# Kernel optimization log

Hardware: AMD Instinct MI355X
Metric: run time of the kernel (lower is better)

## Reference

```python
import jax, jax.numpy as jnp
import numpy as np

B, N, D, U = 8, 2048, 512, 512

def setup_inputs() -> dict:
    key = jax.random.key(0)
    ks = jax.random.split(key, 7)
    s = 1.0 / np.sqrt(D)
    return {
        "inputs": jax.random.normal(ks[0], (B, N, D), dtype=jnp.float32),
        "Wq": jax.random.normal(ks[1], (D, U), dtype=jnp.float32) * s,
        "bq": jnp.zeros((U,), dtype=jnp.float32),
        "Wk": jax.random.normal(ks[2], (D, U), dtype=jnp.float32) * s,
        "bk": jnp.zeros((U,), dtype=jnp.float32),
        "Wv": jax.random.normal(ks[3], (D, U), dtype=jnp.float32) * s,
        "bv": jnp.zeros((U,), dtype=jnp.float32),
    }

def reference(inputs, Wq, bq, Wk, bk, Wv, bv):
    # Dense projections (Keras Dense: x @ W + b)
    Q = inputs @ Wq + bq  # [B, N, U]
    K = inputs @ Wk + bk  # [B, N, U]
    V = inputs @ Wv + bv  # [B, N, U]
    # NOTE: original module has NO 1/sqrt(d) scaling
    scores = jnp.einsum("bnu,bmu->bnm", Q, K)  # [B, N, N]
    attn = jax.nn.softmax(scores, axis=-1)
    return jnp.einsum("bnm,bmu->bnu", attn, V)  # [B, N, U]
```

## Files before the change

### kernel.cpp

```cpp
#include <hip/hip_runtime.h>


typedef _Float16 f16;
typedef _Float16 f16x4 __attribute__((ext_vector_type(4)));
typedef _Float16 f16x8 __attribute__((ext_vector_type(8)));
typedef float f32x4 __attribute__((ext_vector_type(4)));
typedef short s16x8 __attribute__((ext_vector_type(8)));
typedef unsigned short u16;

#define OFS 96.0f

__device__ __forceinline__ void stage16(const void* g, void* lds_uniform) {
    __builtin_amdgcn_global_load_lds(
        (const __attribute__((address_space(1))) void*)g,
        (__attribute__((address_space(3))) void*)lds_uniform,
        16, 0, 0);
}

__device__ __forceinline__ unsigned lds_off(const void* p) {
    return (unsigned)(size_t)(const __attribute__((address_space(3))) void*)p;
}

__device__ __forceinline__ f16x8 dsread16(unsigned a) {
    f16x8 r;
    asm volatile("ds_read_b128 %0, %1" : "=v"(r) : "v"(a));
    return r;
}
__device__ __forceinline__ s16x8 dsread16b(unsigned a) {
    s16x8 r;
    asm volatile("ds_read_b128 %0, %1" : "=v"(r) : "v"(a));
    return r;
}

__device__ __forceinline__ u16 f2bf(float f) {
    unsigned u = __builtin_bit_cast(unsigned, f);
    u = (u + 0x7FFF + ((u >> 16) & 1)) >> 16;
    return (u16)u;
}
__device__ __forceinline__ float bf2f(u16 b) {
    return __builtin_bit_cast(float, (unsigned)b << 16);
}

__global__ __launch_bounds__(256) void prep_fused(
    const float* __restrict__ X,
    const float* __restrict__ Wq, const float* __restrict__ Wk,
    const float* __restrict__ Wv,
    const float* __restrict__ bq, const float* __restrict__ bk,
    const float* __restrict__ bv,
    f16* __restrict__ X16, f16* __restrict__ Wt, float* __restrict__ biases) {
    __shared__ float t[32][33];
    const int bid = blockIdx.x, tid = threadIdx.x;
    if (bid < 8192) {
        int i = (bid * 256 + tid) * 4;
        float4 v = *(const float4*)(X + i);
        f16x4 o;
        o[0] = (f16)v.x; o[1] = (f16)v.y; o[2] = (f16)v.z; o[3] = (f16)v.w;
        *(f16x4*)(X16 + i) = o;
    } else if (bid < 8960) {
        int id = bid - 8192;
        int z = id >> 8, rem = id & 255;
        int u0 = (rem & 15) * 32, d0 = (rem >> 4) * 32;
        const float* W = (z == 0) ? Wq : (z == 1 ? Wk : Wv);
        f16* outp = Wt + (size_t)z * 262144;
        int tx = tid & 31, ty = tid >> 5;
#pragma unroll
        for (int r = 0; r < 4; r++)
            t[ty + 8 * r][tx] = W[(size_t)(d0 + ty + 8 * r) * 512 + u0 + tx];
        __syncthreads();
#pragma unroll
        for (int r = 0; r < 4; r++)
            outp[(size_t)(u0 + ty + 8 * r) * 512 + d0 + tx] = (f16)t[tx][ty + 8 * r];
    } else {
#pragma unroll
        for (int j = 0; j < 6; j++) {
            int i = j * 256 + tid;
            float v = (i < 512) ? bq[i] : (i < 1024) ? bk[i - 512] : bv[i - 1024];
            biases[i] = v;
        }
    }
}

template <int MODE>
__device__ __forceinline__ void gemm_core(
    const u16* __restrict__ A, int lda,
    const u16* __restrict__ Bt, int ldb,
    int m0, int n0, int K,
    const float* __restrict__ bias,
    void* __restrict__ Cv, int ldc,
    u16* As, u16* Bs) {
    __shared__ float rowbuf[128];

    const int tid = threadIdx.x;
    const int wid = tid >> 6, lane = tid & 63;

    if (MODE == 2) {
        if (tid < 128) rowbuf[tid] = bias[m0 + tid];
    }

    const int schunk = (lane & 7) ^ ((lane >> 3) & 7);
    const u16* gA = A + (size_t)(m0 + wid * 32 + (lane >> 3)) * lda + schunk * 8;
    const u16* gB = Bt + (size_t)(n0 + wid * 32 + (lane >> 3)) * ldb + schunk * 8;
    u16* ldsA = As + (wid * 32) * 64;
    u16* ldsB = Bs + (wid * 32) * 64;

    const int wr = wid >> 1, wc = wid & 1;
    const int frow = lane & 15;
    const int f7 = frow & 7;
    const int c_lo = (lane >> 4) ^ f7;
    const int c_hi = ((lane >> 4) | 4) ^ f7;
    const u16* fA_lo = As + (wr * 64 + frow) * 64 + c_lo * 8;
    const u16* fA_hi = As + (wr * 64 + frow) * 64 + c_hi * 8;
    const u16* fB_lo = Bs + (wc * 64 + frow) * 64 + c_lo * 8;
    const u16* fB_hi = Bs + (wc * 64 + frow) * 64 + c_hi * 8;

    f32x4 acc[4][4] = {};

    for (int kt = 0; kt < K; kt += 64) {
#pragma unroll
        for (int j = 0; j < 4; j++)
            stage16(gA + (size_t)(j * 8) * lda, ldsA + (j * 8) * 64);
#pragma unroll
        for (int j = 0; j < 4; j++)
            stage16(gB + (size_t)(j * 8) * ldb, ldsB + (j * 8) * 64);
        gA += 64; gB += 64;
        __syncthreads();

#pragma unroll
        for (int half = 0; half < 2; half++) {
            const u16* pA = half ? fA_hi : fA_lo;
            const u16* pB = half ? fB_hi : fB_lo;
            f16x8 af[4], bf[4];
#pragma unroll
            for (int i = 0; i < 4; i++) af[i] = *(const f16x8*)(const f16*)(pA + i * 16 * 64);
#pragma unroll
            for (int i = 0; i < 4; i++) bf[i] = *(const f16x8*)(const f16*)(pB + i * 16 * 64);
#pragma unroll
            for (int mi = 0; mi < 4; mi++)
#pragma unroll
                for (int ni = 0; ni < 4; ni++)
                    acc[mi][ni] = __builtin_amdgcn_mfma_f32_16x16x32_f16(
                        af[mi], bf[ni], acc[mi][ni], 0, 0, 0);
        }
        __syncthreads();
    }

    const int crow0 = m0 + wr * 64 + ((lane >> 4) << 2);
    const int ccol0 = n0 + wc * 64 + (lane & 15);

    if (MODE == 1) {
        f16* C = (f16*)Cv;
#pragma unroll
        for (int mi = 0; mi < 4; mi++)
#pragma unroll
            for (int ni = 0; ni < 4; ni++) {
                float cb = bias[ccol0 + ni * 16];
#pragma unroll
                for (int r = 0; r < 4; r++)
                    C[(size_t)(crow0 + mi * 16 + r) * ldc + ccol0 + ni * 16] =
                        (f16)(acc[mi][ni][r] + cb);
            }
    } else {
        u16* C = (u16*)Cv;
#pragma unroll
        for (int mi = 0; mi < 4; mi++)
#pragma unroll
            for (int ni = 0; ni < 4; ni++)
#pragma unroll
                for (int r = 0; r < 4; r++) {
                    float rb = rowbuf[crow0 + mi * 16 + r - m0];
                    C[(size_t)(crow0 + mi * 16 + r) * ldc + ccol0 + ni * 16] =
                        f2bf(acc[mi][ni][r] + rb);
                }
    }
}

__global__ __launch_bounds__(256, 3) void proj_fused(
    const u16* __restrict__ X16, const u16* __restrict__ Wt,
    const float* __restrict__ biases,
    u16* __restrict__ QK, u16* __restrict__ Vt) {
    __shared__ __align__(16) u16 As[128 * 64];
    __shared__ __align__(16) u16 Bs[128 * 64];
    const int bid = blockIdx.x;
    if (bid < 1024) {
        int z = bid >> 9, rem = bid & 511;
        int bx = rem & 127, by = rem >> 7;
        gemm_core<1>(X16, 512, Wt + (size_t)z * 262144, 512,
                     bx * 128, by * 128, 512,
                     biases + z * 512,
                     QK + (size_t)z * 8388608, 512, As, Bs);
    } else {
        int id = bid - 1024;
        int bz = id & 7, rem = id >> 3;
        int bx = rem & 3, by = rem >> 2;
        gemm_core<2>(Wt + (size_t)2 * 262144, 512,
                     X16 + (size_t)bz * 1048576, 512,
                     bx * 128, by * 128, 512,
                     biases + 1024,
                     Vt + (size_t)bz * 1048576, 2048, As, Bs);
    }
}

__global__ __launch_bounds__(512, 2) void score_gemm(
    const u16* __restrict__ Q, const u16* __restrict__ Kk,
    u16* __restrict__ P, float* __restrict__ rsp) {
    extern __shared__ __align__(16) char smem[];

    const int i = blockIdx.x;
    const int z = i & 7, y = (i >> 3) & 7, x = i >> 6;
    const int m0 = x * 256, n0 = y * 256;
    const u16* A  = Q  + (size_t)z * 1048576;
    const u16* Bt = Kk + (size_t)z * 1048576;
    u16* C = P + (size_t)z * 4194304;
    float* rs = rsp + ((size_t)z * 8 + y) * 8192;

    const int tid = threadIdx.x;
    const int wid = tid >> 6, lane = tid & 63;

    const int srow = lane >> 3;
    const int schunk = (lane & 7) ^ srow;
    const u16* gA0 = A  + (size_t)m0 * 512 + schunk * 8;
    const u16* gB0 = Bt + (size_t)n0 * 512 + schunk * 8;
    char* ldsbase = smem;

    auto stage_unit = [&](int u, int T, int b) {
        const u16* gm = (u < 2) ? gA0 : gB0;
        int rbase = (u & 1) * 128 + wid * 16;
        const u16* g = gm + (size_t)(rbase + srow) * 512 + T * 64;
        char* l = ldsbase + ((u < 2) ? 0 : 65536) + b * 32768 + rbase * 128;
        stage16(g, l);
        stage16(g + (size_t)8 * 512, l + 8 * 128);
    };

    const int wr = wid >> 2, wc = wid & 3;
    const int frow = lane & 15;
    const int f7 = frow & 7;
    const int c_lo = (lane >> 4) ^ f7;
    const int c_hi = ((lane >> 4) | 4) ^ f7;
    const unsigned smemB = lds_off(smem);
    const unsigned offA_lo = (unsigned)(((wr * 128 + frow) * 64 + c_lo * 8) * 2);
    const unsigned offA_hi = (unsigned)(((wr * 128 + frow) * 64 + c_hi * 8) * 2);
    const unsigned offB_lo = (unsigned)(((wc * 64 + frow) * 64 + c_lo * 8) * 2);
    const unsigned offB_hi = (unsigned)(((wc * 64 + frow) * 64 + c_hi * 8) * 2);

    f32x4 acc[8][4] = {};

    stage_unit(0, 0, 0); stage_unit(1, 0, 0);
    stage_unit(2, 0, 0); stage_unit(3, 0, 0);
    asm volatile("s_waitcnt vmcnt(0)" ::: "memory");
    asm volatile("s_barrier" ::: "memory");

#pragma unroll
    for (int T = 0; T < 8; ++T) {
        const int buf = T & 1;
        const unsigned baseA = smemB + (unsigned)(buf * 32768);
        const unsigned baseB = smemB + 65536u + (unsigned)(buf * 32768);

        f16x8 bf[4];
#pragma unroll
        for (int p = 0; p < 4; ++p) {
            const int kh = p >> 1, mh = p & 1;
            const unsigned aoff = baseA + (kh ? offA_hi : offA_lo);
            if (mh == 0) {
                const unsigned boff = baseB + (kh ? offB_hi : offB_lo);
#pragma unroll
                for (int ni = 0; ni < 4; ni++)
                    bf[ni] = dsread16(boff + (unsigned)(ni * 2048));
            }
            f16x8 af[4];
#pragma unroll
            for (int j = 0; j < 4; j++)
                af[j] = dsread16(aoff + (unsigned)((4 * mh + j) * 2048));

            if (T < 7) {
                if (p == 0) { stage_unit(0, T + 1, buf ^ 1); stage_unit(1, T + 1, buf ^ 1); }
                if (p == 1) { stage_unit(2, T + 1, buf ^ 1); stage_unit(3, T + 1, buf ^ 1); }
            }

            asm volatile("s_waitcnt lgkmcnt(0)" ::: "memory");
            __builtin_amdgcn_sched_barrier(0);
            __builtin_amdgcn_s_setprio(1);
#pragma unroll
            for (int j = 0; j < 4; j++)
#pragma unroll
                for (int ni = 0; ni < 4; ni++)
                    acc[4 * mh + j][ni] = __builtin_amdgcn_mfma_f32_16x16x32_f16(
                        af[j], bf[ni], acc[4 * mh + j][ni], 0, 0, 0);
            __builtin_amdgcn_s_setprio(0);

            if (p == 3)
                asm volatile("s_waitcnt vmcnt(0)" ::: "memory");
            asm volatile("s_barrier" ::: "memory");
        }
    }

    const int crow0 = m0 + wr * 128 + ((lane >> 4) << 2);
    const int ccol0 = n0 + wc * 64 + (lane & 15);
#pragma unroll
    for (int mi = 0; mi < 8; mi++)
#pragma unroll
        for (int r = 0; r < 4; r++) {
            float rsum = 0.0f;
#pragma unroll
            for (int ni = 0; ni < 4; ni++) {
                u16 b = f2bf(__expf(acc[mi][ni][r] - OFS));
                C[(size_t)(crow0 + mi * 16 + r) * 2048 + ccol0 + ni * 16] = b;
                rsum += bf2f(b);
            }
#pragma unroll
            for (int o = 1; o < 16; o <<= 1)
                rsum += __shfl_xor(rsum, o, 64);
            if ((lane & 15) == 0)
                rs[wc * 2048 + crow0 + mi * 16 + r] = rsum;
        }
}

__global__ __launch_bounds__(256, 2) void pv_gemm(
    const u16* __restrict__ P, const u16* __restrict__ Vt,
    const float* __restrict__ rsp, float* __restrict__ out) {
    extern __shared__ __align__(16) char smem[];

    const int i = blockIdx.x;
    const int z = i & 7, y = (i >> 3) & 3, x = i >> 5;
    const int m0 = x * 128, n0 = y * 128;
    const u16* A  = P  + (size_t)z * 4194304;
    const u16* Bt = Vt + (size_t)z * 1048576;
    const float* rs = rsp + (size_t)z * 65536;
    float* C = out + (size_t)z * 1048576;

    const int tid = threadIdx.x;
    const int wid = tid >> 6, lane = tid & 63;

    float* rowbuf = (float*)(smem + 65536);
    if (tid < 128) {
        const float* rp = rs + m0 + tid;
        float s = 0.0f;
#pragma unroll
        for (int p = 0; p < 32; p++) s += rp[p * 2048];
        rowbuf[tid] = s;
    }

    const int schunk = (lane & 7) ^ ((lane >> 3) & 7);
    const u16* gA = A + (size_t)(m0 + wid * 32 + (lane >> 3)) * 2048 + schunk * 8;
    const u16* gB = Bt + (size_t)(n0 + wid * 32 + (lane >> 3)) * 2048 + schunk * 8;
    const int ldsoff = (wid * 32) * 128;

    auto stage_tile = [&](int T, int b) {
        char* dA = smem + b * 16384 + ldsoff;
        char* dB = smem + 32768 + b * 16384 + ldsoff;
#pragma unroll
        for (int j = 0; j < 4; j++)
            stage16(gA + (size_t)(j * 8) * 2048 + T * 64, dA + (j * 8) * 128);
#pragma unroll
        for (int j = 0; j < 4; j++)
            stage16(gB + (size_t)(j * 8) * 2048 + T * 64, dB + (j * 8) * 128);
    };

    const int wr = wid >> 1, wc = wid & 1;
    const int frow = lane & 15;
    const int f7 = frow & 7;
    const int c_lo = (lane >> 4) ^ f7;
    const int c_hi = ((lane >> 4) | 4) ^ f7;
    const unsigned smemB = lds_off(smem);
    const unsigned oA_lo = (unsigned)(((wr * 64 + frow) * 64 + c_lo * 8) * 2);
    const unsigned oA_hi = (unsigned)(((wr * 64 + frow) * 64 + c_hi * 8) * 2);
    const unsigned oB_lo = (unsigned)(((wc * 64 + frow) * 64 + c_lo * 8) * 2);
    const unsigned oB_hi = (unsigned)(((wc * 64 + frow) * 64 + c_hi * 8) * 2);

    f32x4 acc[4][4] = {};

    stage_tile(0, 0);
    asm volatile("s_waitcnt vmcnt(0)" ::: "memory");
    asm volatile("s_barrier" ::: "memory");

#pragma unroll 2
    for (int T = 0; T < 32; ++T) {
        const int buf = T & 1;
        const unsigned aBase = smemB + (unsigned)(buf * 16384);
        const unsigned bBase = smemB + 32768u + (unsigned)(buf * 16384);

#pragma unroll
        for (int kh = 0; kh < 2; ++kh) {
            const unsigned ao = aBase + (kh ? oA_hi : oA_lo);
            const unsigned bo = bBase + (kh ? oB_hi : oB_lo);
            s16x8 af[4], bf[4];
#pragma unroll
            for (int t = 0; t < 4; t++) bf[t] = dsread16b(bo + (unsigned)(t * 2048));
#pragma unroll
            for (int t = 0; t < 4; t++) af[t] = dsread16b(ao + (unsigned)(t * 2048));

            if (kh == 0 && T < 31) stage_tile(T + 1, buf ^ 1);

            asm volatile("s_waitcnt lgkmcnt(0)" ::: "memory");
            __builtin_amdgcn_sched_barrier(0);
            __builtin_amdgcn_s_setprio(1);
#pragma unroll
            for (int mi = 0; mi < 4; mi++)
#pragma unroll
                for (int ni = 0; ni < 4; ni++)
                    acc[mi][ni] = __builtin_amdgcn_mfma_f32_16x16x32_bf16(
                        af[mi], bf[ni], acc[mi][ni], 0, 0, 0);
            __builtin_amdgcn_s_setprio(0);

            if (kh == 1)
                asm volatile("s_waitcnt vmcnt(0)" ::: "memory");
            asm volatile("s_barrier" ::: "memory");
        }
    }

    const int crow0 = m0 + wr * 64 + ((lane >> 4) << 2);
    const int ccol0 = n0 + wc * 64 + (lane & 15);
#pragma unroll
    for (int mi = 0; mi < 4; mi++) {
        float inv[4];
#pragma unroll
        for (int r = 0; r < 4; r++)
            inv[r] = 1.0f / rowbuf[crow0 + mi * 16 + r - m0];
#pragma unroll
        for (int ni = 0; ni < 4; ni++)
#pragma unroll
            for (int r = 0; r < 4; r++)
                C[(size_t)(crow0 + mi * 16 + r) * 512 + ccol0 + ni * 16] =
                    acc[mi][ni][r] * inv[r];
    }
}


extern "C" void kernel_launch(void* const* d_in, const int* in_sizes, int n_in,
                              void* d_out, int out_size, void* d_ws, size_t ws_size,
                              hipStream_t stream) {
    const float* X  = (const float*)d_in[0];
    const float* Wq = (const float*)d_in[1];
    const float* bq = (const float*)d_in[2];
    const float* Wk = (const float*)d_in[3];
    const float* bk = (const float*)d_in[4];
    const float* Wv = (const float*)d_in[5];
    const float* bv = (const float*)d_in[6];
    float* out = (float*)d_out;
    char* ws = (char*)d_ws;

    f16*   X16    = (f16*)ws;
    f16*   Wt     = (f16*)(ws + 16777216);
    float* biases = (float*)(ws + 18350080);
    u16*   QK     = (u16*)(ws + 18356224);
    u16*   Vt     = (u16*)(ws + 51910656);
    u16*   P      = (u16*)(ws + 68687872);
    float* rsp    = (float*)ws;

    static bool s_attr_done = false;
    if (!s_attr_done) {
        (void)hipFuncSetAttribute(reinterpret_cast<const void*>(score_gemm),
                                  hipFuncAttributeMaxDynamicSharedMemorySize,
                                  131072);
        (void)hipFuncSetAttribute(reinterpret_cast<const void*>(pv_gemm),
                                  hipFuncAttributeMaxDynamicSharedMemorySize,
                                  66048);
        s_attr_done = true;
    }

    prep_fused<<<8961, 256, 0, stream>>>(X, Wq, Wk, Wv, bq, bk, bv,
                                         X16, Wt, biases);

    proj_fused<<<1536, 256, 0, stream>>>((const u16*)X16, (const u16*)Wt,
                                         biases, QK, Vt);

    score_gemm<<<512, 512, 131072, stream>>>(QK, QK + (size_t)8388608, P, rsp);

    pv_gemm<<<512, 256, 66048, stream>>>(P, Vt, rsp, out);
}
```

Measured before the change: 203.6 us.

## Double-buffer LDS tiles in projection GEMM to overlap loads with MFMA

Rewrites the projection GEMM core into a software-pipelined loop that prefetches the next K tile into a second LDS buffer while MFMAs run on the current one. It uses explicit waitcnt/barrier placement and raises wave priority around the MFMA block. The aim is to hide global-to-LDS latency that the old single-buffer load-sync-compute-sync loop exposed. LDS use doubles to 64KB per block and occupancy drops from 3 to 2 blocks per CU, which could offset the gain.

```diff
diff --git a/kernel.cpp b/kernel.cpp
--- a/kernel.cpp
+++ b/kernel.cpp
@@ -81,13 +81,10 @@
 }
 
 template <int MODE>
-__device__ __forceinline__ void gemm_core(
-    const u16* __restrict__ A, int lda,
-    const u16* __restrict__ Bt, int ldb,
-    int m0, int n0, int K,
-    const float* __restrict__ bias,
-    void* __restrict__ Cv, int ldc,
-    u16* As, u16* Bs) {
+__device__ __forceinline__ void gemm_pipe(
+    const u16* __restrict__ A, const u16* __restrict__ Bt,
+    int m0, int n0, const float* __restrict__ bias,
+    void* __restrict__ Cv, int ldc, char* smem) {
     __shared__ float rowbuf[128];
 
     const int tid = threadIdx.x;
@@ -98,50 +95,71 @@
     }
 
     const int schunk = (lane & 7) ^ ((lane >> 3) & 7);
-    const u16* gA = A + (size_t)(m0 + wid * 32 + (lane >> 3)) * lda + schunk * 8;
-    const u16* gB = Bt + (size_t)(n0 + wid * 32 + (lane >> 3)) * ldb + schunk * 8;
-    u16* ldsA = As + (wid * 32) * 64;
-    u16* ldsB = Bs + (wid * 32) * 64;
+    const u16* gA = A + (size_t)(m0 + wid * 32 + (lane >> 3)) * 512 + schunk * 8;
+    const u16* gB = Bt + (size_t)(n0 + wid * 32 + (lane >> 3)) * 512 + schunk * 8;
+    const int ldsoff = (wid * 32) * 128;
+
+    auto stage_tile = [&](int T, int b) {
+        char* dA = smem + b * 16384 + ldsoff;
+        char* dB = smem + 32768 + b * 16384 + ldsoff;
+#pragma unroll
+        for (int j = 0; j < 4; j++)
+            stage16(gA + (size_t)(j * 8) * 512 + T * 64, dA + (j * 8) * 128);
+#pragma unroll
+        for (int j = 0; j < 4; j++)
+            stage16(gB + (size_t)(j * 8) * 512 + T * 64, dB + (j * 8) * 128);
+    };
 
     const int wr = wid >> 1, wc = wid & 1;
     const int frow = lane & 15;
     const int f7 = frow & 7;
     const int c_lo = (lane >> 4) ^ f7;
     const int c_hi = ((lane >> 4) | 4) ^ f7;
-    const u16* fA_lo = As + (wr * 64 + frow) * 64 + c_lo * 8;
-    const u16* fA_hi = As + (wr * 64 + frow) * 64 + c_hi * 8;
-    const u16* fB_lo = Bs + (wc * 64 + frow) * 64 + c_lo * 8;
-    const u16* fB_hi = Bs + (wc * 64 + frow) * 64 + c_hi * 8;
+    const unsigned smemB = lds_off(smem);
+    const unsigned oA_lo = (unsigned)(((wr * 64 + frow) * 64 + c_lo * 8) * 2);
+    const unsigned oA_hi = (unsigned)(((wr * 64 + frow) * 64 + c_hi * 8) * 2);
+    const unsigned oB_lo = (unsigned)(((wc * 64 + frow) * 64 + c_lo * 8) * 2);
+    const unsigned oB_hi = (unsigned)(((wc * 64 + frow) * 64 + c_hi * 8) * 2);
 
     f32x4 acc[4][4] = {};
 
-    for (int kt = 0; kt < K; kt += 64) {
-#pragma unroll
-        for (int j = 0; j < 4; j++)
-            stage16(gA + (size_t)(j * 8) * lda, ldsA + (j * 8) * 64);
-#pragma unroll
-        for (int j = 0; j < 4; j++)
-            stage16(gB + (size_t)(j * 8) * ldb, ldsB + (j * 8) * 64);
-        gA += 64; gB += 64;
-        __syncthreads();
-
-#pragma unroll
-        for (int half = 0; half < 2; half++) {
-            const u16* pA = half ? fA_hi : fA_lo;
-            const u16* pB = half ? fB_hi : fB_lo;
+    stage_tile(0, 0);
+    asm volatile("s_waitcnt vmcnt(0)" ::: "memory");
+    asm volatile("s_barrier" ::: "memory");
+
+#pragma unroll
+    for (int T = 0; T < 8; ++T) {
+        const int buf = T & 1;
+        const unsigned aBase = smemB + (unsigned)(buf * 16384);
+        const unsigned bBase = smemB + 32768u + (unsigned)(buf * 16384);
+
+#pragma unroll
+        for (int kh = 0; kh < 2; ++kh) {
+            const unsigned ao = aBase + (kh ? oA_hi : oA_lo);
+            const unsigned bo = bBase + (kh ? oB_hi : oB_lo);
             f16x8 af[4], bf[4];
 #pragma unroll
-            for (int i = 0; i < 4; i++) af[i] = *(const f16x8*)(const f16*)(pA + i * 16 * 64);
-#pragma unroll
-            for (int i = 0; i < 4; i++) bf[i] = *(const f16x8*)(const f16*)(pB + i * 16 * 64);
+            for (int t = 0; t < 4; t++) bf[t] = dsread16(bo + (unsigned)(t * 2048));
+#pragma unroll
+            for (int t = 0; t < 4; t++) af[t] = dsread16(ao + (unsigned)(t * 2048));
+
+            if (kh == 0 && T < 7) stage_tile(T + 1, buf ^ 1);
+
+            asm volatile("s_waitcnt lgkmcnt(0)" ::: "memory");
+            __builtin_amdgcn_sched_barrier(0);
+            __builtin_amdgcn_s_setprio(1);
 #pragma unroll
             for (int mi = 0; mi < 4; mi++)
 #pragma unroll
                 for (int ni = 0; ni < 4; ni++)
                     acc[mi][ni] = __builtin_amdgcn_mfma_f32_16x16x32_f16(
                         af[mi], bf[ni], acc[mi][ni], 0, 0, 0);
+            __builtin_amdgcn_s_setprio(0);
+
+            if (kh == 1)
+                asm volatile("s_waitcnt vmcnt(0)" ::: "memory");
+            asm volatile("s_barrier" ::: "memory");
         }
-        __syncthreads();
     }
 
     const int crow0 = m0 + wr * 64 + ((lane >> 4) << 2);
@@ -174,29 +192,28 @@
     }
 }
 
-__global__ __launch_bounds__(256, 3) void proj_fused(
+__global__ __launch_bounds__(256, 2) void proj_fused(
     const u16* __restrict__ X16, const u16* __restrict__ Wt,
     const float* __restrict__ biases,
     u16* __restrict__ QK, u16* __restrict__ Vt) {
-    __shared__ __align__(16) u16 As[128 * 64];
-    __shared__ __align__(16) u16 Bs[128 * 64];
+    extern __shared__ __align__(16) char smem[];
     const int bid = blockIdx.x;
     if (bid < 1024) {
         int z = bid >> 9, rem = bid & 511;
         int bx = rem & 127, by = rem >> 7;
-        gemm_core<1>(X16, 512, Wt + (size_t)z * 262144, 512,
-                     bx * 128, by * 128, 512,
+        gemm_pipe<1>(X16, Wt + (size_t)z * 262144,
+                     bx * 128, by * 128,
                      biases + z * 512,
-                     QK + (size_t)z * 8388608, 512, As, Bs);
+                     QK + (size_t)z * 8388608, 512, smem);
     } else {
         int id = bid - 1024;
         int bz = id & 7, rem = id >> 3;
         int bx = rem & 3, by = rem >> 2;
-        gemm_core<2>(Wt + (size_t)2 * 262144, 512,
-                     X16 + (size_t)bz * 1048576, 512,
-                     bx * 128, by * 128, 512,
+        gemm_pipe<2>(Wt + (size_t)2 * 262144,
+                     X16 + (size_t)bz * 1048576,
+                     bx * 128, by * 128,
                      biases + 1024,
-                     Vt + (size_t)bz * 1048576, 2048, As, Bs);
+                     Vt + (size_t)bz * 1048576, 2048, smem);
     }
 }
 
@@ -454,14 +471,17 @@
         (void)hipFuncSetAttribute(reinterpret_cast<const void*>(pv_gemm),
                                   hipFuncAttributeMaxDynamicSharedMemorySize,
                                   66048);
+        (void)hipFuncSetAttribute(reinterpret_cast<const void*>(proj_fused),
+                                  hipFuncAttributeMaxDynamicSharedMemorySize,
+                                  65536);
         s_attr_done = true;
     }
 
     prep_fused<<<8961, 256, 0, stream>>>(X, Wq, Wk, Wv, bq, bk, bv,
                                          X16, Wt, biases);
 
-    proj_fused<<<1536, 256, 0, stream>>>((const u16*)X16, (const u16*)Wt,
-                                         biases, QK, Vt);
+    proj_fused<<<1536, 256, 65536, stream>>>((const u16*)X16, (const u16*)Wt,
+                                             biases, QK, Vt);
 
     score_gemm<<<512, 512, 131072, stream>>>(QK, QK + (size_t)8388608, P, rsp);
 
```

Result: no change. 205.1 us (+0.7%).
